# Optimization experiments

Measured on AMD Instinct MI355X. Metric: run time of the kernel, lower is better.

## Reference

```python
import jax, jax.numpy as jnp
import numpy as np

B, L, C = 8, 65536, 64   # Cin must equal filters (broadcast constraint in original code)
F = 64                   # filters
K_ = 3                   # kernel_size
DL = 256                 # latent dim
EPS = 1e-8


def setup_inputs() -> dict:
    key = jax.random.key(0)
    k1, k2, k3, k4 = jax.random.split(key, 4)
    data = jax.random.normal(k1, (B, L, C), dtype=jnp.float32)
    ltnt = jax.random.normal(k2, (B, DL), dtype=jnp.float32)
    # glorot_normal-style scaling for learned params
    kernel = jax.random.normal(k3, (K_, C, F), dtype=jnp.float32) * np.sqrt(2.0 / (C * K_ + F))
    Wd = jax.random.normal(k4, (DL, F), dtype=jnp.float32) * np.sqrt(2.0 / (DL + F))
    bd = jnp.zeros((F,), dtype=jnp.float32)
    return {"data": data, "ltnt": ltnt, "kernel": kernel, "Wd": Wd, "bd": bd}


def reference(data, ltnt, kernel, Wd, bd):
    # per-sample modulation scale from latent: s in [B, F] (F == Cin)
    s = jax.nn.softplus(ltnt @ Wd + bd) + 1.0
    # demodulation: d[b,f] = rsqrt(sum_{k,c} (kernel[k,c,f]*s[b,c])^2 + eps)
    d = jax.lax.rsqrt(jnp.einsum('kcf,bc->bf', kernel * kernel, s * s) + EPS)
    # fused equivalent of per-sample weight modulation:
    #   conv(x, kernel * s[b,c] * d[b,f]) == d[b,f] * conv(x * s[b,c], kernel)
    xm = data * s[:, None, :]                          # [B, L, C]
    y = jax.lax.conv_general_dilated(
        xm, kernel, window_strides=(1,), padding='SAME',
        dimension_numbers=('NWC', 'WIO', 'NWC'))       # [B, L, F]
    return y * d[:, None, :]
```

## Files before the change

### kernel.cpp

```cpp
#include <hip/hip_runtime.h>

#define BATCH 8
#define SEQ   65536
#define CH    64
#define FILT  64
#define DLAT  256
#define TL    64
#define PADW  72

typedef __bf16 bfrag  __attribute__((ext_vector_type(8)));
typedef __bf16 bf16x4 __attribute__((ext_vector_type(4)));
typedef float  floatx4 __attribute__((ext_vector_type(4)));

__global__ __launch_bounds__(256) void prep_kernel(
    const float* __restrict__ ltnt, const float* __restrict__ ker,
    const float* __restrict__ Wd,   const float* __restrict__ bd,
    float* __restrict__ s_ws, float* __restrict__ d_ws, __bf16* __restrict__ kT)
{
    int blk = blockIdx.x;
    int tid = threadIdx.x;
    if (blk < BATCH) {
        int b = blk;
        __shared__ float red[4][64];
        __shared__ float s_sh[64];
        int f = tid & 63, p = tid >> 6;
        float sum = 0.f;
        for (int j = p * 64; j < p * 64 + 64; ++j)
            sum += ltnt[b * DLAT + j] * Wd[j * FILT + f];
        red[p][f] = sum;
        __syncthreads();
        if (tid < 64) {
            float tot = red[0][tid] + red[1][tid] + red[2][tid] + red[3][tid] + bd[tid];
            float sp = (tot > 20.f) ? tot : log1pf(expf(tot));
            float s = sp + 1.f;
            s_ws[b * 64 + tid] = s;
            s_sh[tid] = s;
        }
        __syncthreads();
        float s2 = 0.f;
        for (int k = 0; k < 3; ++k)
            for (int c = p * 16; c < p * 16 + 16; ++c) {
                float w = ker[k * 4096 + c * 64 + f];
                float sc = s_sh[c];
                s2 += w * w * sc * sc;
            }
        __syncthreads();
        red[p][f] = s2;
        __syncthreads();
        if (tid < 64) {
            float tot = red[0][tid] + red[1][tid] + red[2][tid] + red[3][tid];
            d_ws[b * 64 + tid] = rsqrtf(tot + 1e-8f);
        }
    } else {
        int cb = blk - BATCH;
        for (int o = cb * 1536 + tid; o < (cb + 1) * 1536; o += 256) {
            int k = o >> 12, f = (o >> 6) & 63, c = o & 63;
            kT[o] = (__bf16)ker[k * 4096 + c * 64 + f];
        }
    }
}

__global__ __launch_bounds__(256, 4) void conv_kernel(
    const float* __restrict__ data, const float* __restrict__ s_ws,
    const float* __restrict__ d_ws, const __bf16* __restrict__ kT,
    float* __restrict__ out)
{
    __shared__ __bf16 xs[66 * PADW];
    __shared__ __bf16 ks[3 * 64 * PADW];

    int tid = threadIdx.x;
    int b   = blockIdx.x >> 10;
    int t0  = (blockIdx.x & 1023) * TL;

    for (int i = tid; i < 1536; i += 256) {
        int o8 = i * 8;
        int k = o8 >> 12, f = (o8 >> 6) & 63, c = o8 & 63;
        uint4 v = *reinterpret_cast<const uint4*>(kT + o8);
        *reinterpret_cast<uint4*>(&ks[(k * 64 + f) * PADW + c]) = v;
    }

    const float* xb = data + (size_t)b * SEQ * CH;
    const float* sb = s_ws + b * 64;
    for (int i = tid; i < 66 * 16; i += 256) {
        int row = i >> 4;
        int c4  = (i & 15) * 4;
        int g   = t0 - 1 + row;
        float4 v = make_float4(0.f, 0.f, 0.f, 0.f);
        if (g >= 0 && g < SEQ)
            v = *reinterpret_cast<const float4*>(xb + (size_t)g * CH + c4);
        float4 sv = *reinterpret_cast<const float4*>(sb + c4);
        bf16x4 pv;
        pv[0] = (__bf16)(v.x * sv.x);
        pv[1] = (__bf16)(v.y * sv.y);
        pv[2] = (__bf16)(v.z * sv.z);
        pv[3] = (__bf16)(v.w * sv.w);
        *reinterpret_cast<bf16x4*>(&xs[row * PADW + c4]) = pv;
    }
    __syncthreads();

    int wave  = tid >> 6;
    int lane  = tid & 63;
    int m     = lane & 15;
    int q     = lane >> 4;
    int rbase = wave * 16;

    floatx4 acc[4] = {floatx4{0,0,0,0}, floatx4{0,0,0,0},
                      floatx4{0,0,0,0}, floatx4{0,0,0,0}};

    bfrag afr[3][2];
    #pragma unroll
    for (int k = 0; k < 3; ++k)
        #pragma unroll
        for (int chh = 0; chh < 2; ++chh)
            afr[k][chh] = *reinterpret_cast<const bfrag*>(
                &xs[(rbase + k + m) * PADW + chh * 32 + q * 8]);

    #pragma unroll
    for (int nt = 0; nt < 4; ++nt) {
        #pragma unroll
        for (int k = 0; k < 3; ++k) {
            #pragma unroll
            for (int chh = 0; chh < 2; ++chh) {
                bfrag bfr = *reinterpret_cast<const bfrag*>(
                    &ks[(k * 64 + nt * 16 + m) * PADW + chh * 32 + q * 8]);
                acc[nt] = __builtin_amdgcn_mfma_f32_16x16x32_bf16(
                    afr[k][chh], bfr, acc[nt], 0, 0, 0);
            }
        }
    }

    float* ob = out + ((size_t)b * SEQ + t0) * FILT;
    const float* db = d_ws + b * 64;
    #pragma unroll
    for (int nt = 0; nt < 4; ++nt) {
        float dm = db[nt * 16 + m];
        #pragma unroll
        for (int r = 0; r < 4; ++r) {
            int row = rbase + q * 4 + r;
            ob[(size_t)row * FILT + nt * 16 + m] = acc[nt][r] * dm;
        }
    }
}

extern "C" void kernel_launch(void* const* d_in, const int* in_sizes, int n_in,
                              void* d_out, int out_size, void* d_ws, size_t ws_size,
                              hipStream_t stream) {
    const float* data = (const float*)d_in[0];
    const float* ltnt = (const float*)d_in[1];
    const float* ker  = (const float*)d_in[2];
    const float* Wd   = (const float*)d_in[3];
    const float* bd   = (const float*)d_in[4];
    float* out = (float*)d_out;

    float*  s_ws = (float*)d_ws;
    float*  d_wsp = s_ws + 512;
    __bf16* kT   = (__bf16*)((char*)d_ws + 4096);

    prep_kernel<<<16, 256, 0, stream>>>(ltnt, ker, Wd, bd, s_ws, d_wsp, kT);
    conv_kernel<<<BATCH * (SEQ / TL), 256, 0, stream>>>(data, s_ws, d_wsp, kT, out);
}
```

Measured before the change: 278.9 us.

## Fold modulation into per-batch weights and stream A fragments directly from global

The prep kernel now builds per-batch modulated weights (kernel * s * d) in bf16, so the conv no longer scales activations or outputs. The conv kernel drops shared memory and keeps all B fragments in registers. Each wave loads A fragments straight from global memory, prefetching the next 64-row tile in registers while it runs MFMAs on the current one, and writes results with nontemporal stores. Fewer, persistent blocks (2 per CU bound) loop over 16 tiles each. The trade-offs are heavier register pressure, lower occupancy, and duplicated global loads of overlapping halo rows across the three taps.

```diff
diff --git a/kernel.cpp b/kernel.cpp
--- a/kernel.cpp
+++ b/kernel.cpp
@@ -5,139 +5,164 @@
 #define CH    64
 #define FILT  64
 #define DLAT  256
-#define TL    64
-#define PADW  72
 
 typedef __bf16 bfrag  __attribute__((ext_vector_type(8)));
-typedef __bf16 bf16x4 __attribute__((ext_vector_type(4)));
 typedef float  floatx4 __attribute__((ext_vector_type(4)));
 
 __global__ __launch_bounds__(256) void prep_kernel(
     const float* __restrict__ ltnt, const float* __restrict__ ker,
     const float* __restrict__ Wd,   const float* __restrict__ bd,
-    float* __restrict__ s_ws, float* __restrict__ d_ws, __bf16* __restrict__ kT)
+    __bf16* __restrict__ kmod)
 {
-    int blk = blockIdx.x;
-    int tid = threadIdx.x;
-    if (blk < BATCH) {
-        int b = blk;
-        __shared__ float red[4][64];
-        __shared__ float s_sh[64];
-        int f = tid & 63, p = tid >> 6;
-        float sum = 0.f;
-        for (int j = p * 64; j < p * 64 + 64; ++j)
-            sum += ltnt[b * DLAT + j] * Wd[j * FILT + f];
-        red[p][f] = sum;
-        __syncthreads();
-        if (tid < 64) {
-            float tot = red[0][tid] + red[1][tid] + red[2][tid] + red[3][tid] + bd[tid];
-            float sp = (tot > 20.f) ? tot : log1pf(expf(tot));
-            float s = sp + 1.f;
-            s_ws[b * 64 + tid] = s;
-            s_sh[tid] = s;
+    int b = blockIdx.x, tid = threadIdx.x;
+    __shared__ float red[4][64];
+    __shared__ float s_sh[64];
+    __shared__ float d_sh[64];
+    int f = tid & 63, p = tid >> 6;
+
+    float sum = 0.f;
+    #pragma unroll 8
+    for (int j = p * 64; j < p * 64 + 64; ++j)
+        sum += ltnt[b * DLAT + j] * Wd[j * FILT + f];
+    red[p][f] = sum;
+    __syncthreads();
+    if (tid < 64) {
+        float tot = red[0][tid] + red[1][tid] + red[2][tid] + red[3][tid] + bd[tid];
+        float sp = (tot > 20.f) ? tot : log1pf(expf(tot));
+        s_sh[tid] = sp + 1.f;
+    }
+    __syncthreads();
+
+    float s2 = 0.f;
+    for (int k = 0; k < 3; ++k)
+        #pragma unroll
+        for (int c = p * 16; c < p * 16 + 16; ++c) {
+            float w = ker[k * 4096 + c * 64 + f];
+            float sc = s_sh[c];
+            s2 += w * w * sc * sc;
         }
-        __syncthreads();
-        float s2 = 0.f;
-        for (int k = 0; k < 3; ++k)
-            for (int c = p * 16; c < p * 16 + 16; ++c) {
-                float w = ker[k * 4096 + c * 64 + f];
-                float sc = s_sh[c];
-                s2 += w * w * sc * sc;
-            }
-        __syncthreads();
-        red[p][f] = s2;
-        __syncthreads();
-        if (tid < 64) {
-            float tot = red[0][tid] + red[1][tid] + red[2][tid] + red[3][tid];
-            d_ws[b * 64 + tid] = rsqrtf(tot + 1e-8f);
-        }
-    } else {
-        int cb = blk - BATCH;
-        for (int o = cb * 1536 + tid; o < (cb + 1) * 1536; o += 256) {
-            int k = o >> 12, f = (o >> 6) & 63, c = o & 63;
-            kT[o] = (__bf16)ker[k * 4096 + c * 64 + f];
-        }
+    __syncthreads();
+    red[p][f] = s2;
+    __syncthreads();
+    if (tid < 64) {
+        float tot = red[0][tid] + red[1][tid] + red[2][tid] + red[3][tid];
+        d_sh[tid] = rsqrtf(tot + 1e-8f);
+    }
+    __syncthreads();
+
+    for (int o = tid; o < 3 * 64 * 64; o += 256) {
+        int k = o >> 12, ff = (o >> 6) & 63, c = o & 63;
+        kmod[b * 12288 + o] = (__bf16)(ker[k * 4096 + c * 64 + ff] * s_sh[c] * d_sh[ff]);
     }
 }
 
-__global__ __launch_bounds__(256, 4) void conv_kernel(
-    const float* __restrict__ data, const float* __restrict__ s_ws,
-    const float* __restrict__ d_ws, const __bf16* __restrict__ kT,
+struct RawA { float4 v[3][2][2]; };
+
+__device__ __forceinline__ float4 scale4(float4 v, float s) {
+    v.x *= s; v.y *= s; v.z *= s; v.w *= s; return v;
+}
+
+__device__ __forceinline__ RawA loadA(const float* __restrict__ xb,
+                                      int r0, int m, int q) {
+    RawA r;
+    if (r0 >= 1 && r0 <= SEQ - 17) {
+        const float* p = xb + (size_t)(r0 + m - 1) * CH + q * 8;
+        #pragma unroll
+        for (int k = 0; k < 3; ++k)
+            #pragma unroll
+            for (int h = 0; h < 2; ++h) {
+                r.v[k][h][0] = *(const float4*)(p + k * CH + h * 32);
+                r.v[k][h][1] = *(const float4*)(p + k * CH + h * 32 + 4);
+            }
+    } else {
+        #pragma unroll
+        for (int k = 0; k < 3; ++k) {
+            int g = r0 + m - 1 + k;
+            bool ok = (unsigned)g < (unsigned)SEQ;
+            const float* p = xb + (size_t)(ok ? g : 0) * CH + q * 8;
+            float sc = ok ? 1.f : 0.f;
+            #pragma unroll
+            for (int h = 0; h < 2; ++h) {
+                r.v[k][h][0] = scale4(*(const float4*)(p + h * 32), sc);
+                r.v[k][h][1] = scale4(*(const float4*)(p + h * 32 + 4), sc);
+            }
+        }
+    }
+    return r;
+}
+
+__device__ __forceinline__ bfrag cvt8(float4 a, float4 b) {
+    bfrag r;
+    r[0] = (__bf16)a.x; r[1] = (__bf16)a.y; r[2] = (__bf16)a.z; r[3] = (__bf16)a.w;
+    r[4] = (__bf16)b.x; r[5] = (__bf16)b.y; r[6] = (__bf16)b.z; r[7] = (__bf16)b.w;
+    return r;
+}
+
+__global__ __launch_bounds__(256, 2) void conv_kernel(
+    const float* __restrict__ data, const __bf16* __restrict__ kmod,
     float* __restrict__ out)
 {
-    __shared__ __bf16 xs[66 * PADW];
-    __shared__ __bf16 ks[3 * 64 * PADW];
+    int tid  = threadIdx.x;
+    int b    = blockIdx.x >> 6;
+    int blk  = blockIdx.x & 63;
+    int wave = tid >> 6, lane = tid & 63;
+    int m = lane & 15, q = lane >> 4;
 
-    int tid = threadIdx.x;
-    int b   = blockIdx.x >> 10;
-    int t0  = (blockIdx.x & 1023) * TL;
-
-    for (int i = tid; i < 1536; i += 256) {
-        int o8 = i * 8;
-        int k = o8 >> 12, f = (o8 >> 6) & 63, c = o8 & 63;
-        uint4 v = *reinterpret_cast<const uint4*>(kT + o8);
-        *reinterpret_cast<uint4*>(&ks[(k * 64 + f) * PADW + c]) = v;
-    }
+    const __bf16* kb = kmod + b * 12288;
+    bfrag Bf[4][3][2];
+    #pragma unroll
+    for (int nt = 0; nt < 4; ++nt)
+        #pragma unroll
+        for (int k = 0; k < 3; ++k)
+            #pragma unroll
+            for (int h = 0; h < 2; ++h)
+                Bf[nt][k][h] = *(const bfrag*)(kb + (k * 64 + nt * 16 + m) * 64 + h * 32 + q * 8);
 
     const float* xb = data + (size_t)b * SEQ * CH;
-    const float* sb = s_ws + b * 64;
-    for (int i = tid; i < 66 * 16; i += 256) {
-        int row = i >> 4;
-        int c4  = (i & 15) * 4;
-        int g   = t0 - 1 + row;
-        float4 v = make_float4(0.f, 0.f, 0.f, 0.f);
-        if (g >= 0 && g < SEQ)
-            v = *reinterpret_cast<const float4*>(xb + (size_t)g * CH + c4);
-        float4 sv = *reinterpret_cast<const float4*>(sb + c4);
-        bf16x4 pv;
-        pv[0] = (__bf16)(v.x * sv.x);
-        pv[1] = (__bf16)(v.y * sv.y);
-        pv[2] = (__bf16)(v.z * sv.z);
-        pv[3] = (__bf16)(v.w * sv.w);
-        *reinterpret_cast<bf16x4*>(&xs[row * PADW + c4]) = pv;
-    }
-    __syncthreads();
+    float*       ob = out  + (size_t)b * SEQ * FILT;
 
-    int wave  = tid >> 6;
-    int lane  = tid & 63;
-    int m     = lane & 15;
-    int q     = lane >> 4;
-    int rbase = wave * 16;
+    int base = blk * 1024 + wave * 16;
 
-    floatx4 acc[4] = {floatx4{0,0,0,0}, floatx4{0,0,0,0},
-                      floatx4{0,0,0,0}, floatx4{0,0,0,0}};
-
-    bfrag afr[3][2];
+    RawA raw = loadA(xb, base, m, q);
+    bfrag Af[3][2];
     #pragma unroll
     for (int k = 0; k < 3; ++k)
         #pragma unroll
-        for (int chh = 0; chh < 2; ++chh)
-            afr[k][chh] = *reinterpret_cast<const bfrag*>(
-                &xs[(rbase + k + m) * PADW + chh * 32 + q * 8]);
+        for (int h = 0; h < 2; ++h)
+            Af[k][h] = cvt8(raw.v[k][h][0], raw.v[k][h][1]);
 
-    #pragma unroll
-    for (int nt = 0; nt < 4; ++nt) {
+    #pragma unroll 1
+    for (int t = 0; t < 16; ++t) {
+        int r0 = base + t * 64;
+
+        if (t < 15)
+            raw = loadA(xb, r0 + 64, m, q);
+
+        floatx4 acc[4] = {floatx4{0,0,0,0}, floatx4{0,0,0,0},
+                          floatx4{0,0,0,0}, floatx4{0,0,0,0}};
         #pragma unroll
-        for (int k = 0; k < 3; ++k) {
+        for (int nt = 0; nt < 4; ++nt)
             #pragma unroll
-            for (int chh = 0; chh < 2; ++chh) {
-                bfrag bfr = *reinterpret_cast<const bfrag*>(
-                    &ks[(k * 64 + nt * 16 + m) * PADW + chh * 32 + q * 8]);
-                acc[nt] = __builtin_amdgcn_mfma_f32_16x16x32_bf16(
-                    afr[k][chh], bfr, acc[nt], 0, 0, 0);
-            }
-        }
-    }
+            for (int k = 0; k < 3; ++k)
+                #pragma unroll
+                for (int h = 0; h < 2; ++h)
+                    acc[nt] = __builtin_amdgcn_mfma_f32_16x16x32_bf16(
+                        Af[k][h], Bf[nt][k][h], acc[nt], 0, 0, 0);
 
-    float* ob = out + ((size_t)b * SEQ + t0) * FILT;
-    const float* db = d_ws + b * 64;
-    #pragma unroll
-    for (int nt = 0; nt < 4; ++nt) {
-        float dm = db[nt * 16 + m];
+        float* op = ob + (size_t)r0 * FILT;
         #pragma unroll
-        for (int r = 0; r < 4; ++r) {
-            int row = rbase + q * 4 + r;
-            ob[(size_t)row * FILT + nt * 16 + m] = acc[nt][r] * dm;
+        for (int nt = 0; nt < 4; ++nt)
+            #pragma unroll
+            for (int r = 0; r < 4; ++r)
+                __builtin_nontemporal_store(acc[nt][r],
+                    op + (size_t)(q * 4 + r) * FILT + nt * 16 + m);
+
+        if (t < 15) {
+            #pragma unroll
+            for (int k = 0; k < 3; ++k)
+                #pragma unroll
+                for (int h = 0; h < 2; ++h)
+                    Af[k][h] = cvt8(raw.v[k][h][0], raw.v[k][h][1]);
         }
     }
 }
@@ -152,10 +177,8 @@
     const float* bd   = (const float*)d_in[4];
     float* out = (float*)d_out;
 
-    float*  s_ws = (float*)d_ws;
-    float*  d_wsp = s_ws + 512;
-    __bf16* kT   = (__bf16*)((char*)d_ws + 4096);
+    __bf16* kmod = (__bf16*)d_ws;
 
-    prep_kernel<<<16, 256, 0, stream>>>(ltnt, ker, Wd, bd, s_ws, d_wsp, kT);
-    conv_kernel<<<BATCH * (SEQ / TL), 256, 0, stream>>>(data, s_ws, d_wsp, kT, out);
+    prep_kernel<<<BATCH, 256, 0, stream>>>(ltnt, ker, Wd, bd, kmod);
+    conv_kernel<<<BATCH * 64, 256, 0, stream>>>(data, kmod, out);
 }
```

New measurement: 275.9 us. Within noise of the previous version (-1.1%).
